# Optimization experiments

Measured on AMD Instinct MI355X. Metric: run time of the kernel, lower is better.

Reference implementation:

```python
import jax, jax.numpy as jnp
import numpy as np

DIM = 128  # matches init kwarg `dim`; scale = 1/sqrt(dim)


def setup_inputs() -> dict:
    key = jax.random.key(0)
    kq, kk, kv = jax.random.split(key, 3)
    B, S, D = 16, 2048, 128
    return {
        "query": jax.random.normal(kq, (B, S, D), dtype=jnp.float32),
        "key": jax.random.normal(kk, (B, S, D), dtype=jnp.float32),
        "value": jax.random.normal(kv, (B, S, D), dtype=jnp.float32),
    }


def reference(query, key, value):
    # scores = Q K^T / sqrt(dim)  -> [B, S, S]
    scale = 1.0 / np.sqrt(DIM).astype(np.float32)
    scores = jnp.einsum("bqd,bkd->bqk", query, key) * scale
    attn = jax.nn.softmax(scores, axis=-1)
    # context = attn @ V -> [B, S, D]
    return jnp.einsum("bqk,bkd->bqd", attn, value)
```

## Files before the change

### kernel.cpp

```cpp
#include <hip/hip_runtime.h>
#include <hip/hip_bf16.h>

namespace {

constexpr int kS  = 2048;
constexpr int kD  = 128;
constexpr int kKB = 128;
constexpr int kNT = kS / kKB;
constexpr int kChunks = 2048;
constexpr size_t kImgUShorts = (size_t)16 * 16 * kChunks * 8;

typedef __attribute__((ext_vector_type(8)))  short bf16x8;
typedef __attribute__((ext_vector_type(16))) float f32x16;
typedef __attribute__((ext_vector_type(4)))  unsigned int u32x4;

__device__ inline unsigned short f2bf(float f) {
  return __builtin_bit_cast(unsigned short, __float2bfloat16(f));
}
__device__ inline unsigned pk2(float lo, float hi) {
  return (unsigned)f2bf(lo) | ((unsigned)f2bf(hi) << 16);
}
__device__ inline float fexp2(float x) { return __builtin_amdgcn_exp2f(x); }

__device__ inline void gload_lds16(const void* g, void* l) {
  __builtin_amdgcn_global_load_lds(
      (const __attribute__((address_space(1))) unsigned int*)g,
      (__attribute__((address_space(3))) unsigned int*)l, 16, 0, 0);
}

__global__ __launch_bounds__(256)
void convert_kv(const float* __restrict__ K, const float* __restrict__ V,
                unsigned short* __restrict__ Kws, unsigned short* __restrict__ Vws)
{
  const int tid = threadIdx.x;
  const int gid = blockIdx.x & 255;
  const int b = gid >> 4, t = gid & 15;
  if (blockIdx.x < 256) {
    const float* src = K + ((size_t)b * kS + t * kKB) * kD;
    unsigned short* dst = Kws + (size_t)gid * kChunks * 8;
#pragma unroll
    for (int i = 0; i < 8; ++i) {
      const int CH = i * 256 + tid;
      const int k = CH >> 4, s = CH & 15;
      const int d8 = s ^ (k & 15);
      const float* p = src + (size_t)k * kD + d8 * 8;
      float4 a = *reinterpret_cast<const float4*>(p);
      float4 c = *reinterpret_cast<const float4*>(p + 4);
      bf16x8 o;
      o[0] = (short)f2bf(a.x); o[1] = (short)f2bf(a.y);
      o[2] = (short)f2bf(a.z); o[3] = (short)f2bf(a.w);
      o[4] = (short)f2bf(c.x); o[5] = (short)f2bf(c.y);
      o[6] = (short)f2bf(c.z); o[7] = (short)f2bf(c.w);
      *reinterpret_cast<bf16x8*>(dst + (size_t)CH * 8) = o;
    }
  } else {
    __shared__ unsigned short VT[128 * 136];
    const float* src = V + ((size_t)b * kS + t * kKB) * kD;
#pragma unroll
    for (int i = 0; i < 16; ++i) {
      const int idx = i * 256 + tid;
      const int k = idx >> 5, d4 = idx & 31;
      float4 v = *reinterpret_cast<const float4*>(src + (size_t)k * kD + d4 * 4);
      VT[(d4 * 4 + 0) * 136 + k] = f2bf(v.x);
      VT[(d4 * 4 + 1) * 136 + k] = f2bf(v.y);
      VT[(d4 * 4 + 2) * 136 + k] = f2bf(v.z);
      VT[(d4 * 4 + 3) * 136 + k] = f2bf(v.w);
    }
    __syncthreads();
    unsigned short* dst = Vws + (size_t)gid * kChunks * 8;
#pragma unroll
    for (int i = 0; i < 8; ++i) {
      const int CH = i * 256 + tid;
      const int d = CH >> 4, s = CH & 15;
      const int k8 = s ^ (d & 15);
      bf16x8 v = *reinterpret_cast<const bf16x8*>(&VT[d * 136 + k8 * 8]);
      *reinterpret_cast<bf16x8*>(dst + (size_t)CH * 8) = v;
    }
  }
}

__global__ __launch_bounds__(1024, 4)
void attn_fwd(const float* __restrict__ Q,
              const unsigned short* __restrict__ Kws,
              const unsigned short* __restrict__ Vws,
              float* __restrict__ O)
{
  __shared__ __align__(16) unsigned char smem[163840];

  const int tid  = threadIdx.x;
  const int wv   = tid >> 6;
  const int qg   = wv & 3;
  const int ksp  = wv >> 2;
  const int lane = tid & 63;
  const int l31  = lane & 31;
  const int hi   = lane >> 5;
  const int m15  = l31 & 15;

  const int bid   = blockIdx.x;
  const int xcd   = bid & 7;
  const int slot  = bid >> 3;
  const int batch = xcd * 2 + (slot >> 4);
  const int qtile = slot & 15;

  const float* Qb = Q + (size_t)batch * kS * kD;
  float*       Ob = O + (size_t)batch * kS * kD;

  auto stageK = [&](int t, int buf) {
    const size_t base = ((size_t)(batch * 16 + t) * kChunks + wv * 128 + lane) * 8;
    unsigned char* kd = smem + buf * 32768 + wv * 2048;
    gload_lds16(Kws + base,          kd);
    gload_lds16(Kws + base + 64 * 8, kd + 1024);
  };
  auto stageV = [&](int t, int buf) {
    const size_t base = ((size_t)(batch * 16 + t) * kChunks + wv * 128 + lane) * 8;
    unsigned char* vd = smem + 65536 + buf * 32768 + wv * 2048;
    gload_lds16(Vws + base,          vd);
    gload_lds16(Vws + base + 64 * 8, vd + 1024);
  };

  stageK(0, 0); stageV(0, 0); stageK(1, 1);

  constexpr float kQScale = 0.08838834764831845f * 1.4426950408889634f;
  {
    unsigned short* Qsm = reinterpret_cast<unsigned short*>(smem + 131072);
    const float* src = Qb + (size_t)(qtile * 128) * kD;
#pragma unroll
    for (int i = 0; i < 2; ++i) {
      const int idx = i * 1024 + tid;
      const int q = idx >> 4, s = idx & 15;
      const int d8 = s ^ (q & 15);
      const float* p = src + (size_t)q * kD + d8 * 8;
      float4 a = *reinterpret_cast<const float4*>(p);
      float4 b = *reinterpret_cast<const float4*>(p + 4);
      bf16x8 f;
      f[0] = (short)f2bf(a.x * kQScale); f[1] = (short)f2bf(a.y * kQScale);
      f[2] = (short)f2bf(a.z * kQScale); f[3] = (short)f2bf(a.w * kQScale);
      f[4] = (short)f2bf(b.x * kQScale); f[5] = (short)f2bf(b.y * kQScale);
      f[6] = (short)f2bf(b.z * kQScale); f[7] = (short)f2bf(b.w * kQScale);
      *reinterpret_cast<bf16x8*>(&Qsm[(size_t)q * 128 + s * 8]) = f;
    }
  }

  f32x16 acc[4];
#pragma unroll
  for (int dt = 0; dt < 4; ++dt)
#pragma unroll
    for (int r = 0; r < 16; ++r) acc[dt][r] = 0.f;
  float mrun = -1e30f, lrun = 0.f;
  bf16x8 pa0v, pa1v;

  __syncthreads();

  const unsigned short* Ksm = reinterpret_cast<const unsigned short*>(smem);
  const unsigned short* Vsm = reinterpret_cast<const unsigned short*>(smem + 65536);
  const unsigned short* Qsm = reinterpret_cast<const unsigned short*>(smem + 131072);
  const int kRowBase = (ksp * 32 + l31) * 128;
  const int qRowBase = (qg  * 32 + l31) * 128;

  auto qk = [&](int kb) -> f32x16 {
    f32x16 sc;
#pragma unroll
    for (int r = 0; r < 16; ++r) sc[r] = 0.f;
    __builtin_amdgcn_s_setprio(1);
#pragma unroll
    for (int c = 0; c < 8; ++c) {
      const int s = ((c << 1) | hi) ^ m15;
      bf16x8 kf = *reinterpret_cast<const bf16x8*>(&Ksm[kb * 16384 + kRowBase + s * 8]);
      bf16x8 qf = *reinterpret_cast<const bf16x8*>(&Qsm[qRowBase + s * 8]);
      sc = __builtin_amdgcn_mfma_f32_32x32x16_bf16(kf, qf, sc, 0, 0, 0);
    }
    __builtin_amdgcn_s_setprio(0);
    return sc;
  };
  auto treemax = [&](const f32x16& sc) {
    float a0 = fmaxf(fmaxf(sc[0], sc[1]),  fmaxf(sc[2],  sc[3]));
    float a1 = fmaxf(fmaxf(sc[4], sc[5]),  fmaxf(sc[6],  sc[7]));
    float a2 = fmaxf(fmaxf(sc[8], sc[9]),  fmaxf(sc[10], sc[11]));
    float a3 = fmaxf(fmaxf(sc[12], sc[13]), fmaxf(sc[14], sc[15]));
    float mt = fmaxf(fmaxf(a0, a1), fmaxf(a2, a3));
    return fmaxf(mt, __shfl_xor(mt, 32));
  };
  auto pv = [&](int vb) {
    const int s0 = ((ksp << 2) | hi) ^ m15;
    __builtin_amdgcn_s_setprio(1);
#pragma unroll
    for (int dt = 0; dt < 4; ++dt) {
      const int vRow = vb * 16384 + (dt * 32 + l31) * 128;
      bf16x8 vf0 = *reinterpret_cast<const bf16x8*>(&Vsm[vRow + s0 * 8]);
      acc[dt] = __builtin_amdgcn_mfma_f32_32x32x16_bf16(vf0, pa0v, acc[dt], 0, 0, 0);
      bf16x8 vf1 = *reinterpret_cast<const bf16x8*>(&Vsm[vRow + (s0 ^ 2) * 8]);
      acc[dt] = __builtin_amdgcn_mfma_f32_32x32x16_bf16(vf1, pa1v, acc[dt], 0, 0, 0);
    }
    __builtin_amdgcn_s_setprio(0);
  };
  auto pack = [&](const f32x16& p) {
    unsigned a0 = pk2(p[0], p[1]),   a1 = pk2(p[2],  p[3]);
    unsigned a2 = pk2(p[4], p[5]),   a3 = pk2(p[6],  p[7]);
    unsigned b0 = pk2(p[8], p[9]),   b1 = pk2(p[10], p[11]);
    unsigned b2 = pk2(p[12], p[13]), b3 = pk2(p[14], p[15]);
    asm("v_permlane32_swap_b32 %0, %1" : "+v"(a0), "+v"(a2));
    asm("v_permlane32_swap_b32 %0, %1" : "+v"(a1), "+v"(a3));
    asm("v_permlane32_swap_b32 %0, %1" : "+v"(b0), "+v"(b2));
    asm("v_permlane32_swap_b32 %0, %1" : "+v"(b1), "+v"(b3));
    u32x4 w0 = {a0, a1, a2, a3};
    u32x4 w1 = {b0, b1, b2, b3};
    pa0v = __builtin_bit_cast(bf16x8, w0);
    pa1v = __builtin_bit_cast(bf16x8, w1);
  };

  {
    f32x16 sc = qk(0);
    const float mt = treemax(sc);
    mrun = mt;
    float rs = 0.f;
#pragma unroll
    for (int r = 0; r < 16; ++r) { sc[r] = fexp2(sc[r] - mrun); rs += sc[r]; }
    rs += __shfl_xor(rs, 32);
    lrun = rs;
    pack(sc);
  }
  __syncthreads();

  for (int t = 0; t < kNT - 1; ++t) {
    const int kb = (t + 1) & 1, vb = t & 1;
    if (t + 2 < kNT) stageK(t + 2, vb);
    stageV(t + 1, kb);

    f32x16 sc = qk(kb);
    const float mt = treemax(sc);
    const bool need = !__all(mt - mrun <= 8.0f);
    const float mnew = need ? fmaxf(mrun, mt) : mrun;

    pv(vb);

    float rs = 0.f;
#pragma unroll
    for (int r = 0; r < 16; ++r) { sc[r] = fexp2(sc[r] - mnew); rs += sc[r]; }
    rs += __shfl_xor(rs, 32);
    if (need) {
      const float corr = fexp2(mrun - mnew);
      lrun *= corr;
#pragma unroll
      for (int dt = 0; dt < 4; ++dt)
#pragma unroll
        for (int r = 0; r < 16; ++r) acc[dt][r] *= corr;
    }
    lrun += rs;
    mrun = mnew;
    pack(sc);

    __syncthreads();
  }

  pv((kNT - 1) & 1);
  __syncthreads();

  float* scr = reinterpret_cast<float*>(smem);
  float* mls = reinterpret_cast<float*>(smem + 131072);
  auto scrAt = [&](int reg, int q, int d) -> float& {
    return scr[reg * 4096 + q * 128 + (d ^ ((q & 7) << 2))];
  };
  auto mlAt  = [&](int qg_, int ksp_, int w, int q) -> float& {
    return mls[((qg_ * 4 + ksp_) * 2 + w) * 32 + q];
  };
  auto drow = [&](int r) { return (r & 3) + 8 * (r >> 2) + 4 * hi; };

  if (ksp >= 2) {
#pragma unroll
    for (int dt = 0; dt < 4; ++dt)
#pragma unroll
      for (int r = 0; r < 16; ++r)
        scrAt(qg + 4 * (ksp - 2), l31, dt * 32 + drow(r)) = acc[dt][r];
  }
  mlAt(qg, ksp, 0, l31) = mrun;
  mlAt(qg, ksp, 1, l31) = lrun;
  __syncthreads();
  if (ksp < 2) {
    const int p = ksp + 2;
    const float m2 = mlAt(qg, p, 0, l31), l2 = mlAt(qg, p, 1, l31);
    const float mm = fmaxf(mrun, m2);
    const float w1 = fexp2(mrun - mm), w2 = fexp2(m2 - mm);
#pragma unroll
    for (int dt = 0; dt < 4; ++dt)
#pragma unroll
      for (int r = 0; r < 16; ++r)
        acc[dt][r] = acc[dt][r] * w1 + scrAt(qg + 4 * (p - 2), l31, dt * 32 + drow(r)) * w2;
    lrun = lrun * w1 + l2 * w2;
    mrun = mm;
  }
  __syncthreads();
  if (ksp == 1) {
#pragma unroll
    for (int dt = 0; dt < 4; ++dt)
#pragma unroll
      for (int r = 0; r < 16; ++r)
        scrAt(qg, l31, dt * 32 + drow(r)) = acc[dt][r];
    mlAt(qg, 1, 0, l31) = mrun;
    mlAt(qg, 1, 1, l31) = lrun;
  }
  __syncthreads();
  if (ksp == 0) {
    const float m2 = mlAt(qg, 1, 0, l31), l2 = mlAt(qg, 1, 1, l31);
    const float mm = fmaxf(mrun, m2);
    const float w1 = fexp2(mrun - mm), w2 = fexp2(m2 - mm);
    const float inv = 1.0f / (lrun * w1 + l2 * w2);
#pragma unroll
    for (int dt = 0; dt < 4; ++dt)
#pragma unroll
      for (int r = 0; r < 16; ++r) {
        const int d = dt * 32 + drow(r);
        scrAt(qg, l31, d) = (acc[dt][r] * w1 + scrAt(qg, l31, d) * w2) * inv;
      }
  }
  __syncthreads();
  const int krow = tid >> 5, c4 = tid & 31;
#pragma unroll
  for (int i = 0; i < 4; ++i) {
    const int row = i * 32 + krow;
    const int q = row & 31;
    float4 val = *reinterpret_cast<const float4*>(
        &scr[(row >> 5) * 4096 + q * 128 + ((c4 * 4) ^ ((q & 7) << 2))]);
    *reinterpret_cast<float4*>(&Ob[(size_t)(qtile * 128 + row) * kD + c4 * 4]) = val;
  }
}

}

extern "C" void kernel_launch(void* const* d_in, const int* in_sizes, int n_in,
                              void* d_out, int out_size, void* d_ws, size_t ws_size,
                              hipStream_t stream) {
  const float* Q = (const float*)d_in[0];
  const float* K = (const float*)d_in[1];
  const float* V = (const float*)d_in[2];
  float* O = (float*)d_out;
  (void)in_sizes; (void)n_in; (void)out_size; (void)ws_size;

  unsigned short* Kws = (unsigned short*)d_ws;
  unsigned short* Vws = Kws + kImgUShorts;

  hipLaunchKernelGGL(convert_kv, dim3(512), dim3(256), 0, stream, K, V, Kws, Vws);
  hipLaunchKernelGGL(attn_fwd,   dim3(256), dim3(1024), 0, stream, Q, Kws, Vws, O);
}
```

Before: 70.53 us.

## Halve block to 8 waves, each covering 64 keys with Q held in registers

The attention block shrinks from 16 to 8 waves. Each wave now processes two 32-key subtiles per KV tile, and its Q fragments are kept in registers instead of being reread from LDS on every QK step. This removes the Q shared-memory buffer and one level of the cross-wave reduction tree, and halves the number of partial accumulators that must be merged at the end. In exchange, each wave uses more registers (the Q fragments plus two score tiles) and does twice the MFMA work per tile, with fewer waves per CU available to hide latency.

```diff
diff --git a/kernel.cpp b/kernel.cpp
--- a/kernel.cpp
+++ b/kernel.cpp
@@ -79,13 +79,14 @@
   }
 }
 
-__global__ __launch_bounds__(1024, 4)
+__global__ __launch_bounds__(512, 2)
 void attn_fwd(const float* __restrict__ Q,
               const unsigned short* __restrict__ Kws,
               const unsigned short* __restrict__ Vws,
               float* __restrict__ O)
 {
-  __shared__ __align__(16) unsigned char smem[163840];
+  __shared__ __align__(16) unsigned char smem[131072];
+  __shared__ float mls[4 * 2 * 32];
 
   const int tid  = threadIdx.x;
   const int wv   = tid >> 6;
@@ -104,41 +105,40 @@
 
   const float* Qb = Q + (size_t)batch * kS * kD;
   float*       Ob = O + (size_t)batch * kS * kD;
+  const int qrow0 = qtile * 128 + qg * 32;
 
   auto stageK = [&](int t, int buf) {
-    const size_t base = ((size_t)(batch * 16 + t) * kChunks + wv * 128 + lane) * 8;
-    unsigned char* kd = smem + buf * 32768 + wv * 2048;
-    gload_lds16(Kws + base,          kd);
-    gload_lds16(Kws + base + 64 * 8, kd + 1024);
+    const size_t base = ((size_t)(batch * 16 + t) * kChunks + wv * 256 + lane) * 8;
+    unsigned char* kd = smem + buf * 32768 + wv * 4096;
+    gload_lds16(Kws + base,           kd);
+    gload_lds16(Kws + base + 64 * 8,  kd + 1024);
+    gload_lds16(Kws + base + 128 * 8, kd + 2048);
+    gload_lds16(Kws + base + 192 * 8, kd + 3072);
   };
   auto stageV = [&](int t, int buf) {
-    const size_t base = ((size_t)(batch * 16 + t) * kChunks + wv * 128 + lane) * 8;
-    unsigned char* vd = smem + 65536 + buf * 32768 + wv * 2048;
-    gload_lds16(Vws + base,          vd);
-    gload_lds16(Vws + base + 64 * 8, vd + 1024);
+    const size_t base = ((size_t)(batch * 16 + t) * kChunks + wv * 256 + lane) * 8;
+    unsigned char* vd = smem + 65536 + buf * 32768 + wv * 4096;
+    gload_lds16(Vws + base,           vd);
+    gload_lds16(Vws + base + 64 * 8,  vd + 1024);
+    gload_lds16(Vws + base + 128 * 8, vd + 2048);
+    gload_lds16(Vws + base + 192 * 8, vd + 3072);
   };
 
   stageK(0, 0); stageV(0, 0); stageK(1, 1);
 
   constexpr float kQScale = 0.08838834764831845f * 1.4426950408889634f;
-  {
-    unsigned short* Qsm = reinterpret_cast<unsigned short*>(smem + 131072);
-    const float* src = Qb + (size_t)(qtile * 128) * kD;
-#pragma unroll
-    for (int i = 0; i < 2; ++i) {
-      const int idx = i * 1024 + tid;
-      const int q = idx >> 4, s = idx & 15;
-      const int d8 = s ^ (q & 15);
-      const float* p = src + (size_t)q * kD + d8 * 8;
-      float4 a = *reinterpret_cast<const float4*>(p);
-      float4 b = *reinterpret_cast<const float4*>(p + 4);
-      bf16x8 f;
-      f[0] = (short)f2bf(a.x * kQScale); f[1] = (short)f2bf(a.y * kQScale);
-      f[2] = (short)f2bf(a.z * kQScale); f[3] = (short)f2bf(a.w * kQScale);
-      f[4] = (short)f2bf(b.x * kQScale); f[5] = (short)f2bf(b.y * kQScale);
-      f[6] = (short)f2bf(b.z * kQScale); f[7] = (short)f2bf(b.w * kQScale);
-      *reinterpret_cast<bf16x8*>(&Qsm[(size_t)q * 128 + s * 8]) = f;
-    }
+  bf16x8 qf[8];
+#pragma unroll
+  for (int c = 0; c < 8; ++c) {
+    const float* p = Qb + (size_t)(qrow0 + l31) * kD + c * 16 + hi * 8;
+    float4 a = *reinterpret_cast<const float4*>(p);
+    float4 b = *reinterpret_cast<const float4*>(p + 4);
+    bf16x8 f;
+    f[0] = (short)f2bf(a.x * kQScale); f[1] = (short)f2bf(a.y * kQScale);
+    f[2] = (short)f2bf(a.z * kQScale); f[3] = (short)f2bf(a.w * kQScale);
+    f[4] = (short)f2bf(b.x * kQScale); f[5] = (short)f2bf(b.y * kQScale);
+    f[6] = (short)f2bf(b.z * kQScale); f[7] = (short)f2bf(b.w * kQScale);
+    qf[c] = f;
   }
 
   f32x16 acc[4];
@@ -147,53 +147,56 @@
 #pragma unroll
     for (int r = 0; r < 16; ++r) acc[dt][r] = 0.f;
   float mrun = -1e30f, lrun = 0.f;
-  bf16x8 pa0v, pa1v;
+  bf16x8 pa[2][2];
 
   __syncthreads();
 
   const unsigned short* Ksm = reinterpret_cast<const unsigned short*>(smem);
   const unsigned short* Vsm = reinterpret_cast<const unsigned short*>(smem + 65536);
-  const unsigned short* Qsm = reinterpret_cast<const unsigned short*>(smem + 131072);
-  const int kRowBase = (ksp * 32 + l31) * 128;
-  const int qRowBase = (qg  * 32 + l31) * 128;
-
-  auto qk = [&](int kb) -> f32x16 {
-    f32x16 sc;
-#pragma unroll
-    for (int r = 0; r < 16; ++r) sc[r] = 0.f;
+
+  auto qk = [&](int kb, f32x16 sc[2]) {
+#pragma unroll
+    for (int kt = 0; kt < 2; ++kt)
+#pragma unroll
+      for (int r = 0; r < 16; ++r) sc[kt][r] = 0.f;
     __builtin_amdgcn_s_setprio(1);
 #pragma unroll
     for (int c = 0; c < 8; ++c) {
       const int s = ((c << 1) | hi) ^ m15;
-      bf16x8 kf = *reinterpret_cast<const bf16x8*>(&Ksm[kb * 16384 + kRowBase + s * 8]);
-      bf16x8 qf = *reinterpret_cast<const bf16x8*>(&Qsm[qRowBase + s * 8]);
-      sc = __builtin_amdgcn_mfma_f32_32x32x16_bf16(kf, qf, sc, 0, 0, 0);
+#pragma unroll
+      for (int kt = 0; kt < 2; ++kt) {
+        const int row = ksp * 64 + kt * 32 + l31;
+        bf16x8 kf = *reinterpret_cast<const bf16x8*>(&Ksm[kb * 16384 + row * 128 + s * 8]);
+        sc[kt] = __builtin_amdgcn_mfma_f32_32x32x16_bf16(kf, qf[c], sc[kt], 0, 0, 0);
+      }
     }
     __builtin_amdgcn_s_setprio(0);
-    return sc;
-  };
-  auto treemax = [&](const f32x16& sc) {
-    float a0 = fmaxf(fmaxf(sc[0], sc[1]),  fmaxf(sc[2],  sc[3]));
-    float a1 = fmaxf(fmaxf(sc[4], sc[5]),  fmaxf(sc[6],  sc[7]));
-    float a2 = fmaxf(fmaxf(sc[8], sc[9]),  fmaxf(sc[10], sc[11]));
-    float a3 = fmaxf(fmaxf(sc[12], sc[13]), fmaxf(sc[14], sc[15]));
-    float mt = fmaxf(fmaxf(a0, a1), fmaxf(a2, a3));
-    return fmaxf(mt, __shfl_xor(mt, 32));
+  };
+  auto treemax = [&](const f32x16 sc[2]) {
+    float m0 = sc[0][0];
+#pragma unroll
+    for (int r = 1; r < 16; ++r) m0 = fmaxf(m0, sc[0][r]);
+#pragma unroll
+    for (int r = 0; r < 16; ++r) m0 = fmaxf(m0, sc[1][r]);
+    return fmaxf(m0, __shfl_xor(m0, 32));
   };
   auto pv = [&](int vb) {
-    const int s0 = ((ksp << 2) | hi) ^ m15;
     __builtin_amdgcn_s_setprio(1);
 #pragma unroll
     for (int dt = 0; dt < 4; ++dt) {
       const int vRow = vb * 16384 + (dt * 32 + l31) * 128;
-      bf16x8 vf0 = *reinterpret_cast<const bf16x8*>(&Vsm[vRow + s0 * 8]);
-      acc[dt] = __builtin_amdgcn_mfma_f32_32x32x16_bf16(vf0, pa0v, acc[dt], 0, 0, 0);
-      bf16x8 vf1 = *reinterpret_cast<const bf16x8*>(&Vsm[vRow + (s0 ^ 2) * 8]);
-      acc[dt] = __builtin_amdgcn_mfma_f32_32x32x16_bf16(vf1, pa1v, acc[dt], 0, 0, 0);
+#pragma unroll
+      for (int kt = 0; kt < 2; ++kt)
+#pragma unroll
+        for (int ks = 0; ks < 2; ++ks) {
+          const int o = 8 * ksp + 4 * kt + 2 * ks + hi;
+          bf16x8 vf = *reinterpret_cast<const bf16x8*>(&Vsm[vRow + (o ^ m15) * 8]);
+          acc[dt] = __builtin_amdgcn_mfma_f32_32x32x16_bf16(vf, pa[kt][ks], acc[dt], 0, 0, 0);
+        }
     }
     __builtin_amdgcn_s_setprio(0);
   };
-  auto pack = [&](const f32x16& p) {
+  auto pack = [&](const f32x16& p, bf16x8* out) {
     unsigned a0 = pk2(p[0], p[1]),   a1 = pk2(p[2],  p[3]);
     unsigned a2 = pk2(p[4], p[5]),   a3 = pk2(p[6],  p[7]);
     unsigned b0 = pk2(p[8], p[9]),   b1 = pk2(p[10], p[11]);
@@ -204,20 +207,23 @@
     asm("v_permlane32_swap_b32 %0, %1" : "+v"(b1), "+v"(b3));
     u32x4 w0 = {a0, a1, a2, a3};
     u32x4 w1 = {b0, b1, b2, b3};
-    pa0v = __builtin_bit_cast(bf16x8, w0);
-    pa1v = __builtin_bit_cast(bf16x8, w1);
+    out[0] = __builtin_bit_cast(bf16x8, w0);
+    out[1] = __builtin_bit_cast(bf16x8, w1);
   };
 
   {
-    f32x16 sc = qk(0);
-    const float mt = treemax(sc);
-    mrun = mt;
+    f32x16 sc[2];
+    qk(0, sc);
+    mrun = treemax(sc);
     float rs = 0.f;
 #pragma unroll
-    for (int r = 0; r < 16; ++r) { sc[r] = fexp2(sc[r] - mrun); rs += sc[r]; }
+    for (int kt = 0; kt < 2; ++kt)
+#pragma unroll
+      for (int r = 0; r < 16; ++r) { sc[kt][r] = fexp2(sc[kt][r] - mrun); rs += sc[kt][r]; }
     rs += __shfl_xor(rs, 32);
     lrun = rs;
-    pack(sc);
+    pack(sc[0], pa[0]);
+    pack(sc[1], pa[1]);
   }
   __syncthreads();
 
@@ -226,7 +232,8 @@
     if (t + 2 < kNT) stageK(t + 2, vb);
     stageV(t + 1, kb);
 
-    f32x16 sc = qk(kb);
+    f32x16 sc[2];
+    qk(kb, sc);
     const float mt = treemax(sc);
     const bool need = !__all(mt - mrun <= 8.0f);
     const float mnew = need ? fmaxf(mrun, mt) : mrun;
@@ -235,7 +242,9 @@
 
     float rs = 0.f;
 #pragma unroll
-    for (int r = 0; r < 16; ++r) { sc[r] = fexp2(sc[r] - mnew); rs += sc[r]; }
+    for (int kt = 0; kt < 2; ++kt)
+#pragma unroll
+      for (int r = 0; r < 16; ++r) { sc[kt][r] = fexp2(sc[kt][r] - mnew); rs += sc[kt][r]; }
     rs += __shfl_xor(rs, 32);
     if (need) {
       const float corr = fexp2(mrun - mnew);
@@ -247,7 +256,8 @@
     }
     lrun += rs;
     mrun = mnew;
-    pack(sc);
+    pack(sc[0], pa[0]);
+    pack(sc[1], pa[1]);
 
     __syncthreads();
   }
@@ -256,51 +266,24 @@
   __syncthreads();
 
   float* scr = reinterpret_cast<float*>(smem);
-  float* mls = reinterpret_cast<float*>(smem + 131072);
   auto scrAt = [&](int reg, int q, int d) -> float& {
     return scr[reg * 4096 + q * 128 + (d ^ ((q & 7) << 2))];
   };
-  auto mlAt  = [&](int qg_, int ksp_, int w, int q) -> float& {
-    return mls[((qg_ * 4 + ksp_) * 2 + w) * 32 + q];
-  };
   auto drow = [&](int r) { return (r & 3) + 8 * (r >> 2) + 4 * hi; };
 
-  if (ksp >= 2) {
-#pragma unroll
-    for (int dt = 0; dt < 4; ++dt)
-#pragma unroll
-      for (int r = 0; r < 16; ++r)
-        scrAt(qg + 4 * (ksp - 2), l31, dt * 32 + drow(r)) = acc[dt][r];
-  }
-  mlAt(qg, ksp, 0, l31) = mrun;
-  mlAt(qg, ksp, 1, l31) = lrun;
-  __syncthreads();
-  if (ksp < 2) {
-    const int p = ksp + 2;
-    const float m2 = mlAt(qg, p, 0, l31), l2 = mlAt(qg, p, 1, l31);
-    const float mm = fmaxf(mrun, m2);
-    const float w1 = fexp2(mrun - mm), w2 = fexp2(m2 - mm);
-#pragma unroll
-    for (int dt = 0; dt < 4; ++dt)
-#pragma unroll
-      for (int r = 0; r < 16; ++r)
-        acc[dt][r] = acc[dt][r] * w1 + scrAt(qg + 4 * (p - 2), l31, dt * 32 + drow(r)) * w2;
-    lrun = lrun * w1 + l2 * w2;
-    mrun = mm;
-  }
-  __syncthreads();
   if (ksp == 1) {
 #pragma unroll
     for (int dt = 0; dt < 4; ++dt)
 #pragma unroll
       for (int r = 0; r < 16; ++r)
         scrAt(qg, l31, dt * 32 + drow(r)) = acc[dt][r];
-    mlAt(qg, 1, 0, l31) = mrun;
-    mlAt(qg, 1, 1, l31) = lrun;
+    mls[(qg * 2 + 0) * 32 + l31] = mrun;
+    mls[(qg * 2 + 1) * 32 + l31] = lrun;
   }
   __syncthreads();
   if (ksp == 0) {
-    const float m2 = mlAt(qg, 1, 0, l31), l2 = mlAt(qg, 1, 1, l31);
+    const float m2 = mls[(qg * 2 + 0) * 32 + l31];
+    const float l2 = mls[(qg * 2 + 1) * 32 + l31];
     const float mm = fmaxf(mrun, m2);
     const float w1 = fexp2(mrun - mm), w2 = fexp2(m2 - mm);
     const float inv = 1.0f / (lrun * w1 + l2 * w2);
@@ -309,14 +292,15 @@
 #pragma unroll
       for (int r = 0; r < 16; ++r) {
         const int d = dt * 32 + drow(r);
-        scrAt(qg, l31, d) = (acc[dt][r] * w1 + scrAt(qg, l31, d) * w2) * inv;
+        float o1 = scrAt(qg, l31, d);
+        scrAt(qg, l31, d) = (acc[dt][r] * w1 + o1 * w2) * inv;
       }
   }
   __syncthreads();
   const int krow = tid >> 5, c4 = tid & 31;
 #pragma unroll
-  for (int i = 0; i < 4; ++i) {
-    const int row = i * 32 + krow;
+  for (int i = 0; i < 8; ++i) {
+    const int row = i * 16 + krow;
     const int q = row & 31;
     float4 val = *reinterpret_cast<const float4*>(
         &scr[(row >> 5) * 4096 + q * 128 + ((c4 * 4) ^ ((q & 7) << 2))]);
@@ -339,5 +323,5 @@
   unsigned short* Vws = Kws + kImgUShorts;
 
   hipLaunchKernelGGL(convert_kv, dim3(512), dim3(256), 0, stream, K, V, Kws, Vws);
-  hipLaunchKernelGGL(attn_fwd,   dim3(256), dim3(1024), 0, stream, Q, Kws, Vws, O);
-}
+  hipLaunchKernelGGL(attn_fwd,   dim3(256), dim3(512), 0, stream, Q, Kws, Vws, O);
+}
```

Result: faster. 65.11 us (-7.7%).
